# Kernel optimization log

Measured on AMD Instinct MI355X. Metric: run time of the kernel, lower is better.

## Reference

```python
import jax, jax.numpy as jnp
import numpy as np

BETA = 0.25
NUM_SEMANTIC = 8192
EPS = 1e-8  # torch F.normalize / cosine_similarity eps


def _normalize(v, axis=-1):
    n = jnp.linalg.norm(v, axis=axis, keepdims=True)
    return v / jnp.maximum(n, EPS)


def _cos_sim(a, b):
    # faithful to F.cosine_similarity(a, b, dim=-1)
    na = jnp.maximum(jnp.linalg.norm(a, axis=-1), EPS)
    nb = jnp.maximum(jnp.linalg.norm(b, axis=-1), EPS)
    return jnp.sum(a * b, axis=-1) / (na * nb)


def setup_inputs() -> dict:
    key = jax.random.key(0)
    k1, k2, k3 = jax.random.split(key, 3)
    x = jax.random.normal(k1, (8192, 1024), dtype=jnp.float32)
    semantic_embeddings = jax.random.normal(k2, (8192, 1024), dtype=jnp.float32)
    # trunc_normal_(std=0.02) ~ clipped normal; plain scaled normal is a fine init stand-in
    learnable_entries = 0.02 * jax.random.normal(k3, (128, 1024), dtype=jnp.float32)
    return {"x": x, "semantic_embeddings": semantic_embeddings,
            "learnable_entries": learnable_entries}


def reference(x, semantic_embeddings, learnable_entries):
    frozen = _normalize(semantic_embeddings)          # [S, D] (buffer, pre-normalized)
    learned = _normalize(learnable_entries)           # [L, D]
    codebook = jnp.concatenate([frozen, learned], 0)  # [S+L, D]

    xn = _normalize(x)                                # [N, D]
    logits = xn @ codebook.T                          # [N, S+L]
    indices = jnp.argmax(logits, axis=-1)             # [N]
    z_q = codebook[indices]                           # [N, D]
    z_q_st = xn + jax.lax.stop_gradient(z_q - xn)

    is_learnable = (indices >= NUM_SEMANTIC).astype(jnp.float32)
    commitment_loss = jnp.mean(1.0 - _cos_sim(xn, jax.lax.stop_gradient(z_q)))
    per_token = 1.0 - _cos_sim(jax.lax.stop_gradient(xn), z_q)
    vq_loss = jnp.sum(per_token * is_learnable) / (jnp.sum(is_learnable) + 1e-6)
    quant_loss = vq_loss + BETA * commitment_loss

    return logits, indices, z_q, z_q_st, vq_loss, commitment_loss, quant_loss
```

## Files before the change

kernel.cpp:

```cpp
#include <hip/hip_runtime.h>
#include <stdint.h>


#define N_TOK   8192
#define DIM     1024
#define N_SEM   8192
#define N_LEARN 128
#define N_CODE  (N_SEM + N_LEARN)

typedef _Float16 f16;
typedef _Float16 f16x4 __attribute__((ext_vector_type(4)));
typedef _Float16 f16x8 __attribute__((ext_vector_type(8)));
typedef float    f32x4 __attribute__((ext_vector_type(4)));

__global__ __launch_bounds__(256) void k_prep(
    const float* __restrict__ x,   float* __restrict__ invnx,
    f16* __restrict__ xHi,  f16* __restrict__ xLo,
    const float* __restrict__ sem, float* __restrict__ invnb,
    f16* __restrict__ semHi, f16* __restrict__ semLo,
    const float* __restrict__ lrn,
    f16* __restrict__ lrnHi, f16* __restrict__ lrnLo,
    unsigned long long* __restrict__ keys)
{
    const int b = blockIdx.x;
    const int t = threadIdx.x;
    const float* in; float* invn; f16* hi; f16* lo; int row;
    if (b < N_TOK) {
        row = b; in = x; invn = invnx; hi = xHi; lo = xLo;
        if (t == 0) keys[row] = 0ULL;
    } else if (b < N_TOK + N_SEM) {
        row = b - N_TOK; in = sem; invn = invnb; hi = semHi; lo = semLo;
    } else {
        row = b - N_TOK - N_SEM; in = lrn; invn = invnb + N_SEM;
        hi = lrnHi; lo = lrnLo;
    }

    float4 v = ((const float4*)(in + (size_t)row * DIM))[t];
    float ss = v.x*v.x + v.y*v.y + v.z*v.z + v.w*v.w;
    #pragma unroll
    for (int off = 32; off > 0; off >>= 1) ss += __shfl_xor(ss, off);
    __shared__ float red[4];
    if ((t & 63) == 0) red[t >> 6] = ss;

    f16 h0 = (f16)v.x, h1 = (f16)v.y, h2 = (f16)v.z, h3 = (f16)v.w;
    f16x4 hv = {h0, h1, h2, h3};
    f16x4 lv = {(f16)(v.x - (float)h0), (f16)(v.y - (float)h1),
                (f16)(v.z - (float)h2), (f16)(v.w - (float)h3)};
    ((f16x4*)(hi + (size_t)row * DIM))[t] = hv;
    ((f16x4*)(lo + (size_t)row * DIM))[t] = lv;

    __syncthreads();
    if (t == 0) {
        float tot = red[0] + red[1] + red[2] + red[3];
        invn[row] = 1.f / fmaxf(sqrtf(tot), 1e-8f);
    }
}

#define BM 128
#define BN 128
#define BK 32

__device__ __forceinline__ void gload16(const void* g, void* l) {
    __builtin_amdgcn_global_load_lds(
        (const __attribute__((address_space(1))) void*)g,
        (__attribute__((address_space(3))) void*)l, 16, 0, 0);
}

__global__ __launch_bounds__(256) void k_gemm_mfma(
    const f16* __restrict__ xHi,  const f16* __restrict__ xLo,
    const f16* __restrict__ semHi, const f16* __restrict__ semLo,
    const f16* __restrict__ lrnHi, const f16* __restrict__ lrnLo,
    const float* __restrict__ invnx, const float* __restrict__ invnb,
    float* __restrict__ logits, unsigned long long* __restrict__ keys)
{
    __shared__ __align__(16) f16 sAh[2][BM * BK];
    __shared__ __align__(16) f16 sAl[2][BM * BK];
    __shared__ __align__(16) f16 sBh[2][BN * BK];
    __shared__ __align__(16) f16 sBl[2][BN * BK];

    const int t    = threadIdx.x;
    const int lane = t & 63;
    const int wid  = t >> 6;
    const int wm   = (wid >> 1) * 64;
    const int wn   = (wid & 1) * 64;

    const int nwg  = (N_TOK / BM) * (N_CODE / BN);
    const int bid  = blockIdx.y * (N_TOK / BM) + blockIdx.x;
    const int swzb = (bid % 8) * (nwg / 8) + bid / 8;
    const int rb   = swzb % (N_TOK / BM);
    const int cb   = swzb / (N_TOK / BM);
    const int row0 = rb * BM;
    const int col0 = cb * BN;

    const f16* bh; const f16* blo;
    if (col0 < N_SEM) { bh = semHi + (size_t)col0 * DIM;
                        blo = semLo + (size_t)col0 * DIM; }
    else              { bh = lrnHi + (size_t)(col0 - N_SEM) * DIM;
                        blo = lrnLo + (size_t)(col0 - N_SEM) * DIM; }
    const f16* ah  = xHi + (size_t)row0 * DIM;
    const f16* alo = xLo + (size_t)row0 * DIM;

    const int sr = t >> 2;
    const int sc = (t & 3) ^ ((sr >> 1) & 3);
    const size_t g0 = (size_t)sr * DIM + sc * 8;
    const size_t g1 = g0 + (size_t)64 * DIM;

    const int fr  = lane & 15;
    const int fg  = lane >> 4;
    const int swz = fg ^ ((fr >> 1) & 3);

    f32x4 acc[4][4];
    #pragma unroll
    for (int i = 0; i < 4; ++i)
        #pragma unroll
        for (int j = 0; j < 4; ++j) acc[i][j] = (f32x4)0.f;

#define STAGE(bf, k0) do { \
        gload16(ah  + g0 + (k0), &sAh[bf][t * 8]); \
        gload16(ah  + g1 + (k0), &sAh[bf][t * 8 + 2048]); \
        gload16(alo + g0 + (k0), &sAl[bf][t * 8]); \
        gload16(alo + g1 + (k0), &sAl[bf][t * 8 + 2048]); \
        gload16(bh  + g0 + (k0), &sBh[bf][t * 8]); \
        gload16(bh  + g1 + (k0), &sBh[bf][t * 8 + 2048]); \
        gload16(blo + g0 + (k0), &sBl[bf][t * 8]); \
        gload16(blo + g1 + (k0), &sBl[bf][t * 8 + 2048]); \
    } while (0)

    STAGE(0, 0);
    __syncthreads();

    int cur = 0;
    #pragma unroll 1
    for (int k0 = 0; k0 < DIM; k0 += BK) {
        if (k0 + BK < DIM) STAGE(cur ^ 1, k0 + BK);

        f16x8 aH[4], aL[4], bH[4], bL[4];
        #pragma unroll
        for (int f = 0; f < 4; ++f) {
            aH[f] = *(const f16x8*)(&sAh[cur][(wm + f * 16 + fr) * BK + swz * 8]);
            aL[f] = *(const f16x8*)(&sAl[cur][(wm + f * 16 + fr) * BK + swz * 8]);
            bH[f] = *(const f16x8*)(&sBh[cur][(wn + f * 16 + fr) * BK + swz * 8]);
            bL[f] = *(const f16x8*)(&sBl[cur][(wn + f * 16 + fr) * BK + swz * 8]);
        }
        __builtin_amdgcn_s_setprio(1);
        #pragma unroll
        for (int i = 0; i < 4; ++i)
            #pragma unroll
            for (int j = 0; j < 4; ++j) {
                acc[i][j] = __builtin_amdgcn_mfma_f32_16x16x32_f16(aH[i], bH[j], acc[i][j], 0, 0, 0);
                acc[i][j] = __builtin_amdgcn_mfma_f32_16x16x32_f16(aH[i], bL[j], acc[i][j], 0, 0, 0);
                acc[i][j] = __builtin_amdgcn_mfma_f32_16x16x32_f16(aL[i], bH[j], acc[i][j], 0, 0, 0);
            }
        __builtin_amdgcn_s_setprio(0);

        __syncthreads();
        cur ^= 1;
    }
#undef STAGE

    float ibv[4];
    #pragma unroll
    for (int fn = 0; fn < 4; ++fn) ibv[fn] = invnb[col0 + wn + fn * 16 + fr];

    #pragma unroll
    for (int fm = 0; fm < 4; ++fm) {
        #pragma unroll
        for (int reg = 0; reg < 4; ++reg) {
            const int row = row0 + wm + fm * 16 + fg * 4 + reg;
            const float ia = invnx[row];
            float best = -3.4e38f; int bcol = 0;
            float* dst = logits + (size_t)row * N_CODE + col0 + wn + fr;
            #pragma unroll
            for (int fn = 0; fn < 4; ++fn) {
                float v = acc[fm][fn][reg] * (ia * ibv[fn]);
                dst[fn * 16] = v;
                int c = col0 + wn + fn * 16 + fr;
                if (v > best) { best = v; bcol = c; }
            }
            #pragma unroll
            for (int off = 8; off > 0; off >>= 1) {
                float ov = __shfl_xor(best, off);
                int   oc = __shfl_xor(bcol, off);
                if (ov > best || (ov == best && oc < bcol)) { best = ov; bcol = oc; }
            }
            if (fr == 0) {
                unsigned int u = __float_as_uint(best);
                unsigned int s = (u & 0x80000000u) ? ~u : (u | 0x80000000u);
                unsigned long long key = ((unsigned long long)s << 14) |
                                         (unsigned long long)(16383 - bcol);
                atomicMax(keys + row, key);
            }
        }
    }
}

__global__ __launch_bounds__(256) void k_epilogue(
    const float* __restrict__ X,
    const float* __restrict__ SEM,
    const float* __restrict__ LRN,
    const float* __restrict__ invnx,
    const float* __restrict__ invnb,
    const unsigned long long* __restrict__ keys,
    float* __restrict__ o_idx,
    float* __restrict__ o_zq,
    float* __restrict__ o_zst,
    float* __restrict__ perTok)
{
    const int tok = blockIdx.x;
    const int t = threadIdx.x;
    const int col = 16383 - (int)(keys[tok] & 16383ULL);
    const float ix = invnx[tok];
    const float ib = invnb[col];
    const float* crow = (col < N_SEM) ? (SEM + (size_t)col * DIM)
                                      : (LRN + (size_t)(col - N_SEM) * DIM);

    float4 xr = ((const float4*)(X + (size_t)tok * DIM))[t];
    float4 cr = ((const float4*)crow)[t];
    float4 xv; xv.x = xr.x*ix; xv.y = xr.y*ix; xv.z = xr.z*ix; xv.w = xr.w*ix;
    float4 zv; zv.x = cr.x*ib; zv.y = cr.y*ib; zv.z = cr.z*ib; zv.w = cr.w*ib;

    float d  = xv.x*zv.x + xv.y*zv.y + xv.z*zv.z + xv.w*zv.w;
    float nx = xv.x*xv.x + xv.y*xv.y + xv.z*xv.z + xv.w*xv.w;
    float nz = zv.x*zv.x + zv.y*zv.y + zv.z*zv.z + zv.w*zv.w;
    #pragma unroll
    for (int off = 32; off > 0; off >>= 1) {
        d  += __shfl_xor(d, off);
        nx += __shfl_xor(nx, off);
        nz += __shfl_xor(nz, off);
    }
    __shared__ float rd[4], rx[4], rz[4];
    if ((t & 63) == 0) { rd[t>>6] = d; rx[t>>6] = nx; rz[t>>6] = nz; }
    __syncthreads();

    float4 zs;
    zs.x = xv.x + (zv.x - xv.x);
    zs.y = xv.y + (zv.y - xv.y);
    zs.z = xv.z + (zv.z - xv.z);
    zs.w = xv.w + (zv.w - xv.w);
    ((float4*)o_zq)[(size_t)tok * 256 + t] = zv;
    ((float4*)o_zst)[(size_t)tok * 256 + t] = zs;

    if (t == 0) {
        float D  = rd[0]+rd[1]+rd[2]+rd[3];
        float NX = rx[0]+rx[1]+rx[2]+rx[3];
        float NZ = rz[0]+rz[1]+rz[2]+rz[3];
        float cs = D / (fmaxf(sqrtf(NX), 1e-8f) * fmaxf(sqrtf(NZ), 1e-8f));
        o_idx[tok]  = (float)col;
        perTok[tok] = 1.f - cs;
    }
}

__global__ __launch_bounds__(256) void k_final(
    const float* __restrict__ perTok,
    const float* __restrict__ o_idx,
    float* __restrict__ o_scal)
{
    const int t = threadIdx.x;
    float cs = 0.f, vs = 0.f, vc = 0.f;
    for (int i = t; i < N_TOK; i += 256) {
        float p = perTok[i];
        cs += p;
        if (o_idx[i] >= (float)N_SEM) { vs += p; vc += 1.f; }
    }
    #pragma unroll
    for (int off = 32; off > 0; off >>= 1) {
        cs += __shfl_xor(cs, off);
        vs += __shfl_xor(vs, off);
        vc += __shfl_xor(vc, off);
    }
    __shared__ float r0[4], r1[4], r2[4];
    if ((t & 63) == 0) { r0[t>>6] = cs; r1[t>>6] = vs; r2[t>>6] = vc; }
    __syncthreads();
    if (t == 0) {
        float C = r0[0]+r0[1]+r0[2]+r0[3];
        float V = r1[0]+r1[1]+r1[2]+r1[3];
        float K = r2[0]+r2[1]+r2[2]+r2[3];
        float commit = C / (float)N_TOK;
        float vq     = V / (K + 1e-6f);
        o_scal[0] = vq;
        o_scal[1] = commit;
        o_scal[2] = vq + 0.25f * commit;
    }
}

extern "C" void kernel_launch(void* const* d_in, const int* in_sizes, int n_in,
                              void* d_out, int out_size, void* d_ws, size_t ws_size,
                              hipStream_t stream) {
    const float* x   = (const float*)d_in[0];
    const float* sem = (const float*)d_in[1];
    const float* lrn = (const float*)d_in[2];

    float* invnx = (float*)d_ws;
    float* invnb = invnx + N_TOK;
    unsigned long long* keys = (unsigned long long*)(invnb + N_CODE);
    float* perTok = (float*)(keys + N_TOK);
    f16* lrnHi = (f16*)(perTok + N_TOK);
    f16* lrnLo = lrnHi + (size_t)N_LEARN * DIM;

    float* out      = (float*)d_out;
    float* o_logits = out;
    float* o_idx    = o_logits + (size_t)N_TOK * N_CODE;
    float* o_zq     = o_idx + N_TOK;
    float* o_zst    = o_zq + (size_t)N_TOK * DIM;
    float* o_scal   = o_zst + (size_t)N_TOK * DIM;

    f16* xHi   = (f16*)o_zq;
    f16* xLo   = xHi + (size_t)N_TOK * DIM;
    f16* semHi = (f16*)o_zst;
    f16* semLo = semHi + (size_t)N_SEM * DIM;

    k_prep<<<N_TOK + N_SEM + N_LEARN, 256, 0, stream>>>(
        x, invnx, xHi, xLo, sem, invnb, semHi, semLo, lrn, lrnHi, lrnLo, keys);

    dim3 g2(N_TOK / BM, N_CODE / BN);
    k_gemm_mfma<<<g2, 256, 0, stream>>>(xHi, xLo, semHi, semLo, lrnHi, lrnLo,
                                        invnx, invnb, o_logits, keys);

    k_epilogue<<<N_TOK, 256, 0, stream>>>(x, sem, lrn, invnx, invnb, keys,
                                          o_idx, o_zq, o_zst, perTok);
    k_final<<<1, 256, 0, stream>>>(perTok, o_idx, o_scal);
}
```

Before: 877.3 us.

## Enlarge GEMM tiles to 256x256 with 8 waves and phased load/MFMA interleave

The split-fp16 GEMM goes from 128x128 tiles with 4 waves to 256x256 tiles with 8 waves. Each wave now owns a 128x64 sub-tile, which raises arithmetic intensity per LDS and global byte. The K loop is split into four MFMA phases, with the next tile's global->LDS loads issued between them and explicit barriers and waitcnts, so copies overlap compute. The workgroup swizzle is dropped, and the partial last column block (learned entries) is handled by clamping rows and skipping invalid waves. The larger tile doubles LDS and accumulator register use, and the grid becomes 32x33 with a mostly idle final column.

After: 851.3 us. -3.0%, faster.

```diff
diff --git a/kernel.cpp b/kernel.cpp
--- a/kernel.cpp
+++ b/kernel.cpp
@@ -56,8 +56,8 @@
     }
 }
 
-#define BM 128
-#define BN 128
+#define BM 256
+#define BN 256
 #define BK 32
 
 __device__ __forceinline__ void gload16(const void* g, void* l) {
@@ -66,7 +66,7 @@
         (__attribute__((address_space(3))) void*)l, 16, 0, 0);
 }
 
-__global__ __launch_bounds__(256) void k_gemm_mfma(
+__global__ __launch_bounds__(512, 2) void k_gemm_mfma(
     const f16* __restrict__ xHi,  const f16* __restrict__ xLo,
     const f16* __restrict__ semHi, const f16* __restrict__ semLo,
     const f16* __restrict__ lrnHi, const f16* __restrict__ lrnLo,
@@ -81,114 +81,153 @@
     const int t    = threadIdx.x;
     const int lane = t & 63;
     const int wid  = t >> 6;
-    const int wm   = (wid >> 1) * 64;
-    const int wn   = (wid & 1) * 64;
-
-    const int nwg  = (N_TOK / BM) * (N_CODE / BN);
-    const int bid  = blockIdx.y * (N_TOK / BM) + blockIdx.x;
-    const int swzb = (bid % 8) * (nwg / 8) + bid / 8;
-    const int rb   = swzb % (N_TOK / BM);
-    const int cb   = swzb / (N_TOK / BM);
-    const int row0 = rb * BM;
-    const int col0 = cb * BN;
-
-    const f16* bh; const f16* blo;
-    if (col0 < N_SEM) { bh = semHi + (size_t)col0 * DIM;
-                        blo = semLo + (size_t)col0 * DIM; }
-    else              { bh = lrnHi + (size_t)(col0 - N_SEM) * DIM;
-                        blo = lrnLo + (size_t)(col0 - N_SEM) * DIM; }
-    const f16* ah  = xHi + (size_t)row0 * DIM;
-    const f16* alo = xLo + (size_t)row0 * DIM;
-
-    const int sr = t >> 2;
-    const int sc = (t & 3) ^ ((sr >> 1) & 3);
-    const size_t g0 = (size_t)sr * DIM + sc * 8;
-    const size_t g1 = g0 + (size_t)64 * DIM;
-
-    const int fr  = lane & 15;
-    const int fg  = lane >> 4;
-    const int swz = fg ^ ((fr >> 1) & 3);
-
-    f32x4 acc[4][4];
-    #pragma unroll
-    for (int i = 0; i < 4; ++i)
+    const int wm   = (wid >> 2) * 128;
+    const int wn   = (wid & 3) * 64;
+    const int row0 = blockIdx.x * BM;
+    const int col0 = blockIdx.y * BN;
+
+    const f16 *bhB, *blB; int bbase, brMax;
+    if (col0 < N_SEM) { bhB = semHi; blB = semLo; bbase = col0; brMax = 255; }
+    else              { bhB = lrnHi; blB = lrnLo; bbase = 0;    brMax = 127; }
+
+    const int srow = t >> 2;
+    const int sc8  = (((t & 3) ^ ((srow >> 1) & 3))) * 8;
+    const int br1  = (128 + srow > brMax) ? brMax : (128 + srow);
+    const f16* aSh0 = xHi + (size_t)(row0 + srow) * DIM + sc8;
+    const f16* aSh1 = aSh0 + (size_t)128 * DIM;
+    const f16* aSl0 = xLo + (size_t)(row0 + srow) * DIM + sc8;
+    const f16* aSl1 = aSl0 + (size_t)128 * DIM;
+    const f16* bSh0 = bhB + (size_t)(bbase + srow) * DIM + sc8;
+    const f16* bSh1 = bhB + (size_t)(bbase + br1) * DIM + sc8;
+    const f16* bSl0 = blB + (size_t)(bbase + srow) * DIM + sc8;
+    const f16* bSl1 = blB + (size_t)(bbase + br1) * DIM + sc8;
+
+    const int fr   = lane & 15;
+    const int fg   = lane >> 4;
+    const int swz8 = (fg ^ ((fr >> 1) & 3)) * 8;
+
+    f32x4 acc[8][4];
+    #pragma unroll
+    for (int i = 0; i < 8; ++i)
         #pragma unroll
         for (int j = 0; j < 4; ++j) acc[i][j] = (f32x4)0.f;
 
-#define STAGE(bf, k0) do { \
-        gload16(ah  + g0 + (k0), &sAh[bf][t * 8]); \
-        gload16(ah  + g1 + (k0), &sAh[bf][t * 8 + 2048]); \
-        gload16(alo + g0 + (k0), &sAl[bf][t * 8]); \
-        gload16(alo + g1 + (k0), &sAl[bf][t * 8 + 2048]); \
-        gload16(bh  + g0 + (k0), &sBh[bf][t * 8]); \
-        gload16(bh  + g1 + (k0), &sBh[bf][t * 8 + 2048]); \
-        gload16(blo + g0 + (k0), &sBl[bf][t * 8]); \
-        gload16(blo + g1 + (k0), &sBl[bf][t * 8 + 2048]); \
-    } while (0)
-
-    STAGE(0, 0);
-    __syncthreads();
+    f16x8 aH[4], aL[4], bH[2][2], bL[2][2];
+
+#define READ_A(MH) do { \
+    _Pragma("unroll") \
+    for (int f = 0; f < 4; ++f) { \
+        const int r = wm + (MH)*64 + f*16 + fr; \
+        aH[f] = *(const f16x8*)(&sAh[cur][r*32 + swz8]); \
+        aL[f] = *(const f16x8*)(&sAl[cur][r*32 + swz8]); \
+    } } while (0)
+
+#define READ_B(NH) do { \
+    _Pragma("unroll") \
+    for (int g = 0; g < 2; ++g) { \
+        const int r = wn + (NH)*32 + g*16 + fr; \
+        bH[NH][g] = *(const f16x8*)(&sBh[cur][r*32 + swz8]); \
+        bL[NH][g] = *(const f16x8*)(&sBl[cur][r*32 + swz8]); \
+    } } while (0)
+
+#define PH_MFMA(MH, NH) do { \
+    _Pragma("unroll") \
+    for (int f = 0; f < 4; ++f) { \
+        _Pragma("unroll") \
+        for (int g = 0; g < 2; ++g) { \
+            acc[(MH)*4+f][(NH)*2+g] = __builtin_amdgcn_mfma_f32_16x16x32_f16(aH[f], bH[NH][g], acc[(MH)*4+f][(NH)*2+g], 0, 0, 0); \
+            acc[(MH)*4+f][(NH)*2+g] = __builtin_amdgcn_mfma_f32_16x16x32_f16(aH[f], bL[NH][g], acc[(MH)*4+f][(NH)*2+g], 0, 0, 0); \
+            acc[(MH)*4+f][(NH)*2+g] = __builtin_amdgcn_mfma_f32_16x16x32_f16(aL[f], bH[NH][g], acc[(MH)*4+f][(NH)*2+g], 0, 0, 0); \
+        } } } while (0)
+
+#define GLD(ARR, P0, P1, BUF, kk) do { \
+    gload16((P0) + (kk), &ARR[BUF][t * 8]); \
+    gload16((P1) + (kk), &ARR[BUF][4096 + t * 8]); } while (0)
+
+#define LGKM0()  asm volatile("s_waitcnt lgkmcnt(0)" ::: "memory")
+#define VM0()    asm volatile("s_waitcnt vmcnt(0)" ::: "memory")
+#define BAR()    __builtin_amdgcn_s_barrier()
+#define PRIO(n)  __builtin_amdgcn_s_setprio(n)
+
+    GLD(sAh, aSh0, aSh1, 0, 0);
+    GLD(sAl, aSl0, aSl1, 0, 0);
+    GLD(sBh, bSh0, bSh1, 0, 0);
+    GLD(sBl, bSl0, bSl1, 0, 0);
+    VM0();
+    BAR();
 
     int cur = 0;
     #pragma unroll 1
     for (int k0 = 0; k0 < DIM; k0 += BK) {
-        if (k0 + BK < DIM) STAGE(cur ^ 1, k0 + BK);
-
-        f16x8 aH[4], aL[4], bH[4], bL[4];
+        const int  k1  = k0 + BK;
+        const bool pre = (k1 < DIM);
+        const int  nxt = cur ^ 1;
+
+        READ_A(0); READ_B(0);
+        if (pre) GLD(sAh, aSh0, aSh1, nxt, k1);
+        BAR(); LGKM0();
+        PRIO(1); PH_MFMA(0, 0); PRIO(0);
+        BAR();
+
+        READ_B(1);
+        if (pre) { GLD(sAl, aSl0, aSl1, nxt, k1);
+                   gload16(bSh0 + k1, &sBh[nxt][t * 8]); }
+        BAR(); LGKM0();
+        PRIO(1); PH_MFMA(0, 1); PRIO(0);
+        BAR();
+
+        READ_A(1);
+        if (pre) { gload16(bSh1 + k1, &sBh[nxt][4096 + t * 8]);
+                   GLD(sBl, bSl0, bSl1, nxt, k1); }
+        BAR(); LGKM0();
+        PRIO(1); PH_MFMA(1, 0); PRIO(0);
+        BAR();
+
+        PRIO(1); PH_MFMA(1, 1); PRIO(0);
+        VM0();
+        BAR();
+        cur ^= 1;
+    }
+#undef READ_A
+#undef READ_B
+#undef PH_MFMA
+#undef GLD
+
+    const bool wvalid = (col0 + wn + 63) < N_CODE;
+    float ibv[4];
+    #pragma unroll
+    for (int nf = 0; nf < 4; ++nf)
+        ibv[nf] = wvalid ? invnb[col0 + wn + nf * 16 + fr] : 1.f;
+
+    if (wvalid) {
         #pragma unroll
-        for (int f = 0; f < 4; ++f) {
-            aH[f] = *(const f16x8*)(&sAh[cur][(wm + f * 16 + fr) * BK + swz * 8]);
-            aL[f] = *(const f16x8*)(&sAl[cur][(wm + f * 16 + fr) * BK + swz * 8]);
-            bH[f] = *(const f16x8*)(&sBh[cur][(wn + f * 16 + fr) * BK + swz * 8]);
-            bL[f] = *(const f16x8*)(&sBl[cur][(wn + f * 16 + fr) * BK + swz * 8]);
-        }
-        __builtin_amdgcn_s_setprio(1);
-        #pragma unroll
-        for (int i = 0; i < 4; ++i)
+        for (int mf = 0; mf < 8; ++mf) {
             #pragma unroll
-            for (int j = 0; j < 4; ++j) {
-                acc[i][j] = __builtin_amdgcn_mfma_f32_16x16x32_f16(aH[i], bH[j], acc[i][j], 0, 0, 0);
-                acc[i][j] = __builtin_amdgcn_mfma_f32_16x16x32_f16(aH[i], bL[j], acc[i][j], 0, 0, 0);
-                acc[i][j] = __builtin_amdgcn_mfma_f32_16x16x32_f16(aL[i], bH[j], acc[i][j], 0, 0, 0);
-            }
-        __builtin_amdgcn_s_setprio(0);
-
-        __syncthreads();
-        cur ^= 1;
-    }
-#undef STAGE
-
-    float ibv[4];
-    #pragma unroll
-    for (int fn = 0; fn < 4; ++fn) ibv[fn] = invnb[col0 + wn + fn * 16 + fr];
-
-    #pragma unroll
-    for (int fm = 0; fm < 4; ++fm) {
-        #pragma unroll
-        for (int reg = 0; reg < 4; ++reg) {
-            const int row = row0 + wm + fm * 16 + fg * 4 + reg;
-            const float ia = invnx[row];
-            float best = -3.4e38f; int bcol = 0;
-            float* dst = logits + (size_t)row * N_CODE + col0 + wn + fr;
-            #pragma unroll
-            for (int fn = 0; fn < 4; ++fn) {
-                float v = acc[fm][fn][reg] * (ia * ibv[fn]);
-                dst[fn * 16] = v;
-                int c = col0 + wn + fn * 16 + fr;
-                if (v > best) { best = v; bcol = c; }
-            }
-            #pragma unroll
-            for (int off = 8; off > 0; off >>= 1) {
-                float ov = __shfl_xor(best, off);
-                int   oc = __shfl_xor(bcol, off);
-                if (ov > best || (ov == best && oc < bcol)) { best = ov; bcol = oc; }
-            }
-            if (fr == 0) {
-                unsigned int u = __float_as_uint(best);
-                unsigned int s = (u & 0x80000000u) ? ~u : (u | 0x80000000u);
-                unsigned long long key = ((unsigned long long)s << 14) |
-                                         (unsigned long long)(16383 - bcol);
-                atomicMax(keys + row, key);
+            for (int reg = 0; reg < 4; ++reg) {
+                const int row = row0 + wm + mf * 16 + fg * 4 + reg;
+                const float ia = invnx[row];
+                float best = -3.4e38f; int bcol = 0;
+                float* dst = logits + (size_t)row * N_CODE + col0 + wn + fr;
+                #pragma unroll
+                for (int nf = 0; nf < 4; ++nf) {
+                    float v = acc[mf][nf][reg] * (ia * ibv[nf]);
+                    dst[nf * 16] = v;
+                    int c = col0 + wn + nf * 16 + fr;
+                    if (v > best) { best = v; bcol = c; }
+                }
+                #pragma unroll
+                for (int off = 8; off > 0; off >>= 1) {
+                    float ov = __shfl_xor(best, off);
+                    int   oc = __shfl_xor(bcol, off);
+                    if (ov > best || (ov == best && oc < bcol)) { best = ov; bcol = oc; }
+                }
+                if (fr == 0) {
+                    unsigned int u = __float_as_uint(best);
+                    unsigned int s = (u & 0x80000000u) ? ~u : (u | 0x80000000u);
+                    unsigned long long key = ((unsigned long long)s << 14) |
+                                             (unsigned long long)(16383 - bcol);
+                    atomicMax(keys + row, key);
+                }
             }
         }
     }
@@ -312,8 +351,8 @@
     k_prep<<<N_TOK + N_SEM + N_LEARN, 256, 0, stream>>>(
         x, invnx, xHi, xLo, sem, invnb, semHi, semLo, lrn, lrnHi, lrnLo, keys);
 
-    dim3 g2(N_TOK / BM, N_CODE / BN);
-    k_gemm_mfma<<<g2, 256, 0, stream>>>(xHi, xLo, semHi, semLo, lrnHi, lrnLo,
+    dim3 g2(N_TOK / BM, (N_CODE + BN - 1) / BN);
+    k_gemm_mfma<<<g2, 512, 0, stream>>>(xHi, xLo, semHi, semLo, lrnHi, lrnLo,
                                         invnx, invnb, o_logits, keys);
 
     k_epilogue<<<N_TOK, 256, 0, stream>>>(x, sem, lrn, invnx, invnb, keys,
```
